# Kernel tuning notes

Measured on AMD Instinct MI355X. Metric: run time of the kernel, lower is better.

Reference implementation:

```python
import jax, jax.numpy as jnp
import numpy as np

N = 100000   # nodes
E = 1200000  # edges (avg degree 12)
F = 64       # hidden features

def setup_inputs() -> dict:
    key = jax.random.key(0)
    ks = jax.random.split(key, 10)
    x = jax.random.normal(ks[0], (N, F), dtype=jnp.float32)
    edge_src = jax.random.randint(ks[1], (E,), 0, N)
    edge_dst = jax.random.randint(ks[2], (E,), 0, N)
    edge_weights = jax.random.uniform(ks[3], (E,), dtype=jnp.float32)
    s = 1.0 / np.sqrt(F)
    W0 = jax.random.normal(ks[4], (F, F), dtype=jnp.float32) * s
    b0 = jnp.zeros((F,), dtype=jnp.float32)
    W1 = jax.random.normal(ks[5], (F, F), dtype=jnp.float32) * s
    b1 = jnp.zeros((F,), dtype=jnp.float32)
    W2 = jax.random.normal(ks[6], (F, 1), dtype=jnp.float32) * s
    b2 = jnp.zeros((1,), dtype=jnp.float32)
    return {"x": x, "edge_src": edge_src, "edge_dst": edge_dst,
            "edge_weights": edge_weights,
            "W0": W0, "b0": b0, "W1": W1, "b1": b1, "W2": W2, "b2": b2}

def reference(x, edge_src, edge_dst, edge_weights, W0, b0, W1, b1, W2, b2):
    n = x.shape[0]
    # GCN symmetric normalization with self loops (weight 1.0), as in pyg.nn.GCNConv
    deg = jax.ops.segment_sum(edge_weights, edge_dst, num_segments=n) + 1.0
    dinv = jax.lax.rsqrt(deg)                       # [N]
    norm = dinv[edge_src] * edge_weights * dinv[edge_dst]  # [E]
    self_norm = dinv * dinv                          # [N], self-loop coefficient

    def conv(h, W, b):
        h = h @ W                                    # linear transform first (PyG order)
        msg = h[edge_src] * norm[:, None]            # [E, F'] gather + scale
        agg = jax.ops.segment_sum(msg, edge_dst, num_segments=n)
        return agg + h * self_norm[:, None] + b

    h = jax.nn.relu(conv(x, W0, b0))
    h = jax.nn.relu(conv(h, W1, b1))
    h = conv(h, W2, b2)                              # [N, 1], no activation on last conv
    return jnp.squeeze(h)                            # [N]
```

## Files before the change

kernel.cpp:

```cpp
#include <hip/hip_runtime.h>

#define NN 100000
#define NE 1200000
#define FF 64
#define NBIN 512
#define BIN_NODES 196
#define BINCAP 2752
#define NTILE 6250
#define TPW 2

using bf16x8 = __attribute__((ext_vector_type(8))) short;
using f32x4  = __attribute__((ext_vector_type(4))) float;

__device__ __forceinline__ unsigned short f2bf(float x) {
    unsigned u = __float_as_uint(x);
    unsigned r = u + 0x7fffu + ((u >> 16) & 1u);
    return (unsigned short)(r >> 16);
}
__device__ __forceinline__ unsigned pack_bf2(float lo, float hi) {
    return (unsigned)f2bf(lo) | ((unsigned)f2bf(hi) << 16);
}
__device__ __forceinline__ float bf2f_lo(unsigned v) {
    return __uint_as_float(v << 16);
}
__device__ __forceinline__ float bf2f_hi(unsigned v) {
    return __uint_as_float(v & 0xffff0000u);
}

__global__ void zero_gptr(int* gptr) {
    gptr[threadIdx.x] = 0;
}

__global__ __launch_bounds__(1024) void bin_edges(
        const int* __restrict__ esrc, const int* __restrict__ edst,
        const float* __restrict__ ew, int* gptr, int2* __restrict__ binbuf, int e) {
    __shared__ int lcnt[NBIN];
    __shared__ int lbase[NBIN];
    int tid = threadIdx.x;
    int per = (e + (int)gridDim.x - 1) / (int)gridDim.x;
    int lo = blockIdx.x * per;
    int hi = min(lo + per, e);

    if (tid < NBIN) lcnt[tid] = 0;
    __syncthreads();

    for (int i = lo + tid; i < hi; i += 1024) {
        int b = (int)((unsigned)edst[i] / BIN_NODES);
        atomicAdd(&lcnt[b], 1);
    }
    __syncthreads();

    if (tid < NBIN) {
        int c = lcnt[tid];
        lbase[tid] = (c > 0) ? atomicAdd(&gptr[tid], c) : 0;
        lcnt[tid] = 0;
    }
    __syncthreads();

    for (int i = lo + tid; i < hi; i += 1024) {
        int d = edst[i];
        int b = (int)((unsigned)d / BIN_NODES);
        int s = atomicAdd(&lcnt[b], 1);
        int pos = lbase[b] + s;
        if (pos < BINCAP)
            binbuf[(size_t)b * BINCAP + pos] =
                make_int2(esrc[i] | ((d - b * BIN_NODES) << 17),
                          __float_as_int(ew[i]));
    }
}

__global__ __launch_bounds__(512) void build_compact(
        const int* __restrict__ gptr, const int2* __restrict__ binbuf,
        const float* __restrict__ x, int2* __restrict__ bucket,
        int* __restrict__ meta, float* __restrict__ dinv,
        uint4* __restrict__ t0, int n) {
    __shared__ int2  lbuck[BINCAP];
    __shared__ int   lc[BIN_NODES];
    __shared__ int   loff[BIN_NODES];
    __shared__ float ldeg[BIN_NODES];
    __shared__ int   sc[256];
    int b = blockIdx.x, tid = threadIdx.x;

    for (int i = tid; i < BIN_NODES; i += 512) { lc[i] = 0; ldeg[i] = 0.0f; }
    __syncthreads();

    int ce = min(gptr[b], BINCAP);
    const int2* bb = binbuf + (size_t)b * BINCAP;

    for (int i = tid; i < ce; i += 512) {
        int2 r = bb[i];
        int ln = (unsigned)r.x >> 17;
        atomicAdd(&lc[ln], 1);
        atomicAdd(&ldeg[ln], __int_as_float(r.y));
    }
    __syncthreads();

    if (tid < 256) sc[tid] = (tid < BIN_NODES) ? ((lc[tid] + 1) & ~1) : 0;
    __syncthreads();
#pragma unroll
    for (int s = 1; s < 256; s <<= 1) {
        int v = (tid < 256 && tid >= s) ? sc[tid - s] : 0;
        __syncthreads();
        if (tid < 256) sc[tid] += v;
        __syncthreads();
    }
    if (tid < BIN_NODES) loff[tid] = sc[tid] - ((lc[tid] + 1) & ~1);
    __syncthreads();
    int total = sc[BIN_NODES - 1];

    for (int i = tid; i < total; i += 512) lbuck[i] = make_int2(0, 0);
    __syncthreads();
    if (tid < BIN_NODES) lc[tid] = loff[tid];
    __syncthreads();

    for (int i = tid; i < ce; i += 512) {
        int2 r = bb[i];
        int ln = (unsigned)r.x >> 17;
        int pos = atomicAdd(&lc[ln], 1);
        lbuck[pos] = make_int2(r.x & 0x1FFFF, r.y);
    }
    __syncthreads();

    int gbase = b * BIN_NODES;
    for (int i = tid; i < BIN_NODES; i += 512) {
        float di = rsqrtf(ldeg[i] + 1.0f);
        int g = gbase + i;
        if (g < n) {
            dinv[g] = di;
            meta[g] = loff[i] | ((sc[i] - loff[i]) << 16);
        }
        ldeg[i] = di;
    }
    __syncthreads();

    {
        int lim4 = total >> 1;
        const int4* s4 = (const int4*)lbuck;
        int4* d4 = (int4*)(bucket + (size_t)b * BINCAP);
        for (int i = tid; i < lim4; i += 512) d4[i] = s4[i];
    }

    int eg = tid >> 3, l = tid & 7;
    for (int i = eg; i < BIN_NODES; i += 64) {
        int g = gbase + i;
        if (g >= n) continue;
        float di = ldeg[i];
        const float4* xp = (const float4*)(x + (size_t)g * FF + l * 8);
        float4 v0 = xp[0], v1 = xp[1];
        uint4 o;
        o.x = pack_bf2(v0.x * di, v0.y * di);
        o.y = pack_bf2(v0.z * di, v0.w * di);
        o.z = pack_bf2(v1.x * di, v1.y * di);
        o.w = pack_bf2(v1.z * di, v1.w * di);
        t0[(size_t)g * 8 + l] = o;
    }
}

__global__ __launch_bounds__(256) void agg8(
        const int* __restrict__ meta, const int4* __restrict__ bucket4,
        const uint4* __restrict__ t, const float* __restrict__ dinv,
        uint4* __restrict__ zb, int n) {
    int node = blockIdx.x * 32 + (threadIdx.x >> 3);
    int l = threadIdx.x & 7;
    if (node >= n) return;

    uint4 sv = t[node * 8 + l];
    float a0 = bf2f_lo(sv.x), a1 = bf2f_hi(sv.x);
    float a2 = bf2f_lo(sv.y), a3 = bf2f_hi(sv.y);
    float a4 = bf2f_lo(sv.z), a5 = bf2f_hi(sv.z);
    float a6 = bf2f_lo(sv.w), a7 = bf2f_hi(sv.w);

    int m = meta[node];
    int c = m >> 16;
    int bin = (int)((unsigned)node / BIN_NODES);
    const int4* bp = bucket4 + (((size_t)bin * BINCAP + (m & 0xFFFF)) >> 1);
    int p = 0;
    for (; p + 3 < c; p += 4) {
        int4 q0 = bp[(p >> 1) + 0];
        int4 q1 = bp[(p >> 1) + 1];
        uint4 v0 = t[q0.x * 8 + l];
        uint4 v1 = t[q0.z * 8 + l];
        uint4 v2 = t[q1.x * 8 + l];
        uint4 v3 = t[q1.z * 8 + l];
        float w0 = __int_as_float(q0.y), w1 = __int_as_float(q0.w);
        float w2 = __int_as_float(q1.y), w3 = __int_as_float(q1.w);
        a0 = fmaf(w0, bf2f_lo(v0.x), a0); a1 = fmaf(w0, bf2f_hi(v0.x), a1);
        a2 = fmaf(w0, bf2f_lo(v0.y), a2); a3 = fmaf(w0, bf2f_hi(v0.y), a3);
        a4 = fmaf(w0, bf2f_lo(v0.z), a4); a5 = fmaf(w0, bf2f_hi(v0.z), a5);
        a6 = fmaf(w0, bf2f_lo(v0.w), a6); a7 = fmaf(w0, bf2f_hi(v0.w), a7);
        a0 = fmaf(w1, bf2f_lo(v1.x), a0); a1 = fmaf(w1, bf2f_hi(v1.x), a1);
        a2 = fmaf(w1, bf2f_lo(v1.y), a2); a3 = fmaf(w1, bf2f_hi(v1.y), a3);
        a4 = fmaf(w1, bf2f_lo(v1.z), a4); a5 = fmaf(w1, bf2f_hi(v1.z), a5);
        a6 = fmaf(w1, bf2f_lo(v1.w), a6); a7 = fmaf(w1, bf2f_hi(v1.w), a7);
        a0 = fmaf(w2, bf2f_lo(v2.x), a0); a1 = fmaf(w2, bf2f_hi(v2.x), a1);
        a2 = fmaf(w2, bf2f_lo(v2.y), a2); a3 = fmaf(w2, bf2f_hi(v2.y), a3);
        a4 = fmaf(w2, bf2f_lo(v2.z), a4); a5 = fmaf(w2, bf2f_hi(v2.z), a5);
        a6 = fmaf(w2, bf2f_lo(v2.w), a6); a7 = fmaf(w2, bf2f_hi(v2.w), a7);
        a0 = fmaf(w3, bf2f_lo(v3.x), a0); a1 = fmaf(w3, bf2f_hi(v3.x), a1);
        a2 = fmaf(w3, bf2f_lo(v3.y), a2); a3 = fmaf(w3, bf2f_hi(v3.y), a3);
        a4 = fmaf(w3, bf2f_lo(v3.z), a4); a5 = fmaf(w3, bf2f_hi(v3.z), a5);
        a6 = fmaf(w3, bf2f_lo(v3.w), a6); a7 = fmaf(w3, bf2f_hi(v3.w), a7);
    }
    if (p < c) {
        int4 q0 = bp[p >> 1];
        uint4 v0 = t[q0.x * 8 + l];
        uint4 v1 = t[q0.z * 8 + l];
        float w0 = __int_as_float(q0.y), w1 = __int_as_float(q0.w);
        a0 = fmaf(w0, bf2f_lo(v0.x), a0); a1 = fmaf(w0, bf2f_hi(v0.x), a1);
        a2 = fmaf(w0, bf2f_lo(v0.y), a2); a3 = fmaf(w0, bf2f_hi(v0.y), a3);
        a4 = fmaf(w0, bf2f_lo(v0.z), a4); a5 = fmaf(w0, bf2f_hi(v0.z), a5);
        a6 = fmaf(w0, bf2f_lo(v0.w), a6); a7 = fmaf(w0, bf2f_hi(v0.w), a7);
        a0 = fmaf(w1, bf2f_lo(v1.x), a0); a1 = fmaf(w1, bf2f_hi(v1.x), a1);
        a2 = fmaf(w1, bf2f_lo(v1.y), a2); a3 = fmaf(w1, bf2f_hi(v1.y), a3);
        a4 = fmaf(w1, bf2f_lo(v1.z), a4); a5 = fmaf(w1, bf2f_hi(v1.z), a5);
        a6 = fmaf(w1, bf2f_lo(v1.w), a6); a7 = fmaf(w1, bf2f_hi(v1.w), a7);
    }
    float di = dinv[node];
    uint4 o;
    o.x = pack_bf2(a0 * di, a1 * di);
    o.y = pack_bf2(a2 * di, a3 * di);
    o.z = pack_bf2(a4 * di, a5 * di);
    o.w = pack_bf2(a6 * di, a7 * di);
    zb[node * 8 + l] = o;
}

__global__ __launch_bounds__(256) void gemmA(
        const unsigned short* __restrict__ zb, const float* __restrict__ W,
        const float* __restrict__ b, const float* __restrict__ dinv,
        unsigned short* __restrict__ t1, int ntiles) {
    int wid = blockIdx.x * 4 + (threadIdx.x >> 6);
    int lane = threadIdx.x & 63;
    int l16 = lane & 15, lg = lane >> 4;

    bf16x8 bf[4][2];
#pragma unroll
    for (int ct = 0; ct < 4; ++ct)
#pragma unroll
        for (int kh = 0; kh < 2; ++kh) {
            bf16x8 f;
#pragma unroll
            for (int j = 0; j < 8; ++j) {
                int k = kh * 32 + lg * 8 + j;
                f[j] = (short)f2bf(W[k * FF + ct * 16 + l16]);
            }
            bf[ct][kh] = f;
        }
    float bias_[4];
#pragma unroll
    for (int ct = 0; ct < 4; ++ct) bias_[ct] = b[ct * 16 + l16];

#pragma unroll
    for (int t = 0; t < TPW; ++t) {
        int tile = wid * TPW + t;
        if (tile >= ntiles) return;
        int rowbase = tile * 16;

        const bf16x8* zr = (const bf16x8*)(zb + (size_t)(rowbase + l16) * FF);
        bf16x8 a0 = zr[lg];
        bf16x8 a1 = zr[lg + 4];

        f32x4 acc[4];
#pragma unroll
        for (int ct = 0; ct < 4; ++ct) {
            acc[ct] = (f32x4){0.f, 0.f, 0.f, 0.f};
            acc[ct] = __builtin_amdgcn_mfma_f32_16x16x32_bf16(a0, bf[ct][0], acc[ct], 0, 0, 0);
            acc[ct] = __builtin_amdgcn_mfma_f32_16x16x32_bf16(a1, bf[ct][1], acc[ct], 0, 0, 0);
        }

        float dv[4];
#pragma unroll
        for (int r = 0; r < 4; ++r) dv[r] = dinv[rowbase + lg * 4 + r];
#pragma unroll
        for (int ct = 0; ct < 4; ++ct)
#pragma unroll
            for (int r = 0; r < 4; ++r) {
                float h = fmaxf(acc[ct][r] + bias_[ct], 0.0f) * dv[r];
                t1[(size_t)(rowbase + lg * 4 + r) * FF + ct * 16 + l16] = f2bf(h);
            }
    }
}

__global__ __launch_bounds__(256) void gemmB_tail(
        const unsigned short* __restrict__ zb, const float* __restrict__ W1,
        const float* __restrict__ b1, const float* __restrict__ W2,
        const float* __restrict__ dinv, float* __restrict__ t3, int ntiles) {
    int wid = blockIdx.x * 4 + (threadIdx.x >> 6);
    int lane = threadIdx.x & 63;
    int l16 = lane & 15, lg = lane >> 4;

    bf16x8 bf[4][2];
#pragma unroll
    for (int ct = 0; ct < 4; ++ct)
#pragma unroll
        for (int kh = 0; kh < 2; ++kh) {
            bf16x8 f;
#pragma unroll
            for (int j = 0; j < 8; ++j) {
                int k = kh * 32 + lg * 8 + j;
                f[j] = (short)f2bf(W1[k * FF + ct * 16 + l16]);
            }
            bf[ct][kh] = f;
        }
    float bias_[4], w2_[4];
#pragma unroll
    for (int ct = 0; ct < 4; ++ct) {
        bias_[ct] = b1[ct * 16 + l16];
        w2_[ct] = W2[ct * 16 + l16];
    }

#pragma unroll
    for (int t = 0; t < TPW; ++t) {
        int tile = wid * TPW + t;
        if (tile >= ntiles) return;
        int rowbase = tile * 16;

        const bf16x8* zr = (const bf16x8*)(zb + (size_t)(rowbase + l16) * FF);
        bf16x8 a0 = zr[lg];
        bf16x8 a1 = zr[lg + 4];

        f32x4 acc[4];
#pragma unroll
        for (int ct = 0; ct < 4; ++ct) {
            acc[ct] = (f32x4){0.f, 0.f, 0.f, 0.f};
            acc[ct] = __builtin_amdgcn_mfma_f32_16x16x32_bf16(a0, bf[ct][0], acc[ct], 0, 0, 0);
            acc[ct] = __builtin_amdgcn_mfma_f32_16x16x32_bf16(a1, bf[ct][1], acc[ct], 0, 0, 0);
        }

        float pr[4];
#pragma unroll
        for (int r = 0; r < 4; ++r) pr[r] = 0.0f;
#pragma unroll
        for (int ct = 0; ct < 4; ++ct)
#pragma unroll
            for (int r = 0; r < 4; ++r)
                pr[r] = fmaf(fmaxf(acc[ct][r] + bias_[ct], 0.0f), w2_[ct], pr[r]);
#pragma unroll
        for (int r = 0; r < 4; ++r) {
            pr[r] += __shfl_xor(pr[r], 1, 64);
            pr[r] += __shfl_xor(pr[r], 2, 64);
            pr[r] += __shfl_xor(pr[r], 4, 64);
            pr[r] += __shfl_xor(pr[r], 8, 64);
        }
        if (l16 == 0) {
#pragma unroll
            for (int r = 0; r < 4; ++r) {
                int row = rowbase + lg * 4 + r;
                t3[row] = pr[r] * dinv[row];
            }
        }
    }
}

__global__ __launch_bounds__(256) void final_out(
        const int* __restrict__ meta, const int2* __restrict__ bucket,
        const float* __restrict__ t3, const float* __restrict__ dinv,
        const float* __restrict__ b2, float* __restrict__ out, int n) {
    int node = blockIdx.x * 4 + (threadIdx.x >> 6);
    int lane = threadIdx.x & 63;
    if (node >= n) return;
    int m = meta[node];
    int c = m >> 16;
    int bin = (int)((unsigned)node / BIN_NODES);
    const int2* bp = bucket + (size_t)bin * BINCAP + (m & 0xFFFF);
    float v = 0.0f;
    for (int p = lane; p < c; p += 64) {
        int2 ed = bp[p];
        v = fmaf(__int_as_float(ed.y), t3[ed.x], v);
    }
#pragma unroll
    for (int off = 1; off < 64; off <<= 1) v += __shfl_xor(v, off, 64);
    if (lane == 0) out[node] = (v + t3[node]) * dinv[node] + b2[0];
}

extern "C" void kernel_launch(void* const* d_in, const int* in_sizes, int n_in,
                              void* d_out, int out_size, void* d_ws, size_t ws_size,
                              hipStream_t stream) {
    const float* x  = (const float*)d_in[0];
    const int* esrc = (const int*)d_in[1];
    const int* edst = (const int*)d_in[2];
    const float* ew = (const float*)d_in[3];
    const float* W0 = (const float*)d_in[4];
    const float* b0 = (const float*)d_in[5];
    const float* W1 = (const float*)d_in[6];
    const float* b1 = (const float*)d_in[7];
    const float* W2 = (const float*)d_in[8];
    const float* b2 = (const float*)d_in[9];
    float* out = (float*)d_out;

    const int n = NN, e = NE;

    char* ws = (char*)d_ws;
    size_t off = 0;
    auto alloc = [&](size_t bytes) {
        char* p = ws + off;
        off += (bytes + 255) & ~size_t(255);
        return p;
    };
    int*   meta   = (int*)  alloc(size_t(n) * 4);
    float* dinv   = (float*)alloc(size_t(n) * 4);
    float* t3     = (float*)alloc(size_t(n) * 4);
    int*   gptr   = (int*)  alloc(size_t(NBIN) * 4);
    int2*  bucket = (int2*) alloc(size_t(NBIN) * BINCAP * 8);
    unsigned short* zbuf = (unsigned short*)alloc(size_t(n) * FF * 2);
    unsigned short* t0   = (unsigned short*)alloc(size_t(n) * FF * 2);
    (void)ws_size;

    int2* binbuf = (int2*)zbuf;
    unsigned short* t1 = t0;

    int gN4  = (n + 3) / 4;
    int gN32 = (n + 31) / 32;
    int gGemm = ((NTILE + TPW - 1) / TPW + 3) / 4;

    zero_gptr<<<1, NBIN, 0, stream>>>(gptr);
    bin_edges<<<256, 1024, 0, stream>>>(esrc, edst, ew, gptr, binbuf, e);
    build_compact<<<NBIN, 512, 0, stream>>>(gptr, binbuf, x, bucket, meta, dinv,
                                            (uint4*)t0, n);
    agg8<<<gN32, 256, 0, stream>>>(meta, (const int4*)bucket, (const uint4*)t0,
                                   dinv, (uint4*)zbuf, n);
    gemmA<<<gGemm, 256, 0, stream>>>(zbuf, W0, b0, dinv, t1, NTILE);
    agg8<<<gN32, 256, 0, stream>>>(meta, (const int4*)bucket, (const uint4*)t1,
                                   dinv, (uint4*)zbuf, n);
    gemmB_tail<<<gGemm, 256, 0, stream>>>(zbuf, W1, b1, W2, dinv, t3, NTILE);
    final_out<<<gN4, 256, 0, stream>>>(meta, (const int2*)bucket, t3, dinv, b2, out, n);
}
```

Before: 134.3 us.

## Fuse neighbor aggregation with MFMA GEMM via shared-memory staging per block

```diff
diff --git a/kernel.cpp b/kernel.cpp
--- a/kernel.cpp
+++ b/kernel.cpp
@@ -6,8 +6,7 @@
 #define NBIN 512
 #define BIN_NODES 196
 #define BINCAP 2752
-#define NTILE 6250
-#define TPW 2
+#define LSTR 9
 
 using bf16x8 = __attribute__((ext_vector_type(8))) short;
 using f32x4  = __attribute__((ext_vector_type(4))) float;
@@ -156,15 +155,11 @@
     }
 }
 
-__global__ __launch_bounds__(256) void agg8(
+__device__ __forceinline__ void agg_node(
         const int* __restrict__ meta, const int4* __restrict__ bucket4,
         const uint4* __restrict__ t, const float* __restrict__ dinv,
-        uint4* __restrict__ zb, int n) {
-    int node = blockIdx.x * 32 + (threadIdx.x >> 3);
-    int l = threadIdx.x & 7;
-    if (node >= n) return;
-
-    uint4 sv = t[node * 8 + l];
+        int node, int l, uint4* __restrict__ ldsrow) {
+    uint4 sv = t[(size_t)node * 8 + l];
     float a0 = bf2f_lo(sv.x), a1 = bf2f_hi(sv.x);
     float a2 = bf2f_lo(sv.y), a3 = bf2f_hi(sv.y);
     float a4 = bf2f_lo(sv.z), a5 = bf2f_hi(sv.z);
@@ -221,132 +216,102 @@
     o.y = pack_bf2(a2 * di, a3 * di);
     o.z = pack_bf2(a4 * di, a5 * di);
     o.w = pack_bf2(a6 * di, a7 * di);
-    zb[node * 8 + l] = o;
-}
-
-__global__ __launch_bounds__(256) void gemmA(
-        const unsigned short* __restrict__ zb, const float* __restrict__ W,
-        const float* __restrict__ b, const float* __restrict__ dinv,
-        unsigned short* __restrict__ t1, int ntiles) {
-    int wid = blockIdx.x * 4 + (threadIdx.x >> 6);
-    int lane = threadIdx.x & 63;
+    ldsrow[l] = o;
+}
+
+__global__ __launch_bounds__(256) void fused_aggA(
+        const int* __restrict__ meta, const int4* __restrict__ bucket4,
+        const uint4* __restrict__ t, const float* __restrict__ dinv,
+        const float* __restrict__ W, const float* __restrict__ b,
+        unsigned short* __restrict__ t1) {
+    __shared__ uint4 lds[32 * LSTR];
+    int tid = threadIdx.x;
+    int r = tid >> 3, l = tid & 7;
+    int nodebase = blockIdx.x * 32;
+    agg_node(meta, bucket4, t, dinv, nodebase + r, l, &lds[r * LSTR]);
+    __syncthreads();
+
+    int wid = tid >> 6, lane = tid & 63;
+    if (wid >= 2) return;
     int l16 = lane & 15, lg = lane >> 4;
-
-    bf16x8 bf[4][2];
-#pragma unroll
-    for (int ct = 0; ct < 4; ++ct)
-#pragma unroll
-        for (int kh = 0; kh < 2; ++kh) {
-            bf16x8 f;
-#pragma unroll
-            for (int j = 0; j < 8; ++j) {
-                int k = kh * 32 + lg * 8 + j;
-                f[j] = (short)f2bf(W[k * FF + ct * 16 + l16]);
-            }
-            bf[ct][kh] = f;
-        }
-    float bias_[4];
-#pragma unroll
-    for (int ct = 0; ct < 4; ++ct) bias_[ct] = b[ct * 16 + l16];
-
-#pragma unroll
-    for (int t = 0; t < TPW; ++t) {
-        int tile = wid * TPW + t;
-        if (tile >= ntiles) return;
-        int rowbase = tile * 16;
-
-        const bf16x8* zr = (const bf16x8*)(zb + (size_t)(rowbase + l16) * FF);
-        bf16x8 a0 = zr[lg];
-        bf16x8 a1 = zr[lg + 4];
-
-        f32x4 acc[4];
-#pragma unroll
-        for (int ct = 0; ct < 4; ++ct) {
-            acc[ct] = (f32x4){0.f, 0.f, 0.f, 0.f};
-            acc[ct] = __builtin_amdgcn_mfma_f32_16x16x32_bf16(a0, bf[ct][0], acc[ct], 0, 0, 0);
-            acc[ct] = __builtin_amdgcn_mfma_f32_16x16x32_bf16(a1, bf[ct][1], acc[ct], 0, 0, 0);
-        }
-
-        float dv[4];
-#pragma unroll
-        for (int r = 0; r < 4; ++r) dv[r] = dinv[rowbase + lg * 4 + r];
-#pragma unroll
-        for (int ct = 0; ct < 4; ++ct)
-#pragma unroll
-            for (int r = 0; r < 4; ++r) {
-                float h = fmaxf(acc[ct][r] + bias_[ct], 0.0f) * dv[r];
-                t1[(size_t)(rowbase + lg * 4 + r) * FF + ct * 16 + l16] = f2bf(h);
-            }
-    }
-}
-
-__global__ __launch_bounds__(256) void gemmB_tail(
-        const unsigned short* __restrict__ zb, const float* __restrict__ W1,
-        const float* __restrict__ b1, const float* __restrict__ W2,
-        const float* __restrict__ dinv, float* __restrict__ t3, int ntiles) {
-    int wid = blockIdx.x * 4 + (threadIdx.x >> 6);
-    int lane = threadIdx.x & 63;
+    int rloc = wid * 16 + l16;
+    int rowbase = nodebase + wid * 16;
+
+    bf16x8 a0 = *(const bf16x8*)&lds[rloc * LSTR + lg];
+    bf16x8 a1 = *(const bf16x8*)&lds[rloc * LSTR + lg + 4];
+
+#pragma unroll
+    for (int ct = 0; ct < 4; ++ct) {
+        bf16x8 bf0, bf1;
+#pragma unroll
+        for (int j = 0; j < 8; ++j) {
+            bf0[j] = (short)f2bf(W[(lg * 8 + j) * FF + ct * 16 + l16]);
+            bf1[j] = (short)f2bf(W[(32 + lg * 8 + j) * FF + ct * 16 + l16]);
+        }
+        f32x4 acc = (f32x4){0.f, 0.f, 0.f, 0.f};
+        acc = __builtin_amdgcn_mfma_f32_16x16x32_bf16(a0, bf0, acc, 0, 0, 0);
+        acc = __builtin_amdgcn_mfma_f32_16x16x32_bf16(a1, bf1, acc, 0, 0, 0);
+        float bias_ = b[ct * 16 + l16];
+#pragma unroll
+        for (int rr = 0; rr < 4; ++rr) {
+            int row = rowbase + lg * 4 + rr;
+            float h = fmaxf(acc[rr] + bias_, 0.0f) * dinv[row];
+            t1[(size_t)row * FF + ct * 16 + l16] = f2bf(h);
+        }
+    }
+}
+
+__global__ __launch_bounds__(256) void fused_aggB(
+        const int* __restrict__ meta, const int4* __restrict__ bucket4,
+        const uint4* __restrict__ t, const float* __restrict__ dinv,
+        const float* __restrict__ W1, const float* __restrict__ b1,
+        const float* __restrict__ W2, float* __restrict__ t3) {
+    __shared__ uint4 lds[32 * LSTR];
+    int tid = threadIdx.x;
+    int r = tid >> 3, l = tid & 7;
+    int nodebase = blockIdx.x * 32;
+    agg_node(meta, bucket4, t, dinv, nodebase + r, l, &lds[r * LSTR]);
+    __syncthreads();
+
+    int wid = tid >> 6, lane = tid & 63;
+    if (wid >= 2) return;
     int l16 = lane & 15, lg = lane >> 4;
-
-    bf16x8 bf[4][2];
-#pragma unroll
-    for (int ct = 0; ct < 4; ++ct)
-#pragma unroll
-        for (int kh = 0; kh < 2; ++kh) {
-            bf16x8 f;
-#pragma unroll
-            for (int j = 0; j < 8; ++j) {
-                int k = kh * 32 + lg * 8 + j;
-                f[j] = (short)f2bf(W1[k * FF + ct * 16 + l16]);
-            }
-            bf[ct][kh] = f;
-        }
-    float bias_[4], w2_[4];
+    int rloc = wid * 16 + l16;
+    int rowbase = nodebase + wid * 16;
+
+    bf16x8 a0 = *(const bf16x8*)&lds[rloc * LSTR + lg];
+    bf16x8 a1 = *(const bf16x8*)&lds[rloc * LSTR + lg + 4];
+
+    float pr[4] = {0.f, 0.f, 0.f, 0.f};
 #pragma unroll
     for (int ct = 0; ct < 4; ++ct) {
-        bias_[ct] = b1[ct * 16 + l16];
-        w2_[ct] = W2[ct * 16 + l16];
-    }
-
-#pragma unroll
-    for (int t = 0; t < TPW; ++t) {
-        int tile = wid * TPW + t;
-        if (tile >= ntiles) return;
-        int rowbase = tile * 16;
-
-        const bf16x8* zr = (const bf16x8*)(zb + (size_t)(rowbase + l16) * FF);
-        bf16x8 a0 = zr[lg];
-        bf16x8 a1 = zr[lg + 4];
-
-        f32x4 acc[4];
-#pragma unroll
-        for (int ct = 0; ct < 4; ++ct) {
-            acc[ct] = (f32x4){0.f, 0.f, 0.f, 0.f};
-            acc[ct] = __builtin_amdgcn_mfma_f32_16x16x32_bf16(a0, bf[ct][0], acc[ct], 0, 0, 0);
-            acc[ct] = __builtin_amdgcn_mfma_f32_16x16x32_bf16(a1, bf[ct][1], acc[ct], 0, 0, 0);
-        }
-
-        float pr[4];
-#pragma unroll
-        for (int r = 0; r < 4; ++r) pr[r] = 0.0f;
-#pragma unroll
-        for (int ct = 0; ct < 4; ++ct)
-#pragma unroll
-            for (int r = 0; r < 4; ++r)
-                pr[r] = fmaf(fmaxf(acc[ct][r] + bias_[ct], 0.0f), w2_[ct], pr[r]);
-#pragma unroll
-        for (int r = 0; r < 4; ++r) {
-            pr[r] += __shfl_xor(pr[r], 1, 64);
-            pr[r] += __shfl_xor(pr[r], 2, 64);
-            pr[r] += __shfl_xor(pr[r], 4, 64);
-            pr[r] += __shfl_xor(pr[r], 8, 64);
-        }
-        if (l16 == 0) {
-#pragma unroll
-            for (int r = 0; r < 4; ++r) {
-                int row = rowbase + lg * 4 + r;
-                t3[row] = pr[r] * dinv[row];
-            }
+        bf16x8 bf0, bf1;
+#pragma unroll
+        for (int j = 0; j < 8; ++j) {
+            bf0[j] = (short)f2bf(W1[(lg * 8 + j) * FF + ct * 16 + l16]);
+            bf1[j] = (short)f2bf(W1[(32 + lg * 8 + j) * FF + ct * 16 + l16]);
+        }
+        f32x4 acc = (f32x4){0.f, 0.f, 0.f, 0.f};
+        acc = __builtin_amdgcn_mfma_f32_16x16x32_bf16(a0, bf0, acc, 0, 0, 0);
+        acc = __builtin_amdgcn_mfma_f32_16x16x32_bf16(a1, bf1, acc, 0, 0, 0);
+        float bias_ = b1[ct * 16 + l16];
+        float w2_ = W2[ct * 16 + l16];
+#pragma unroll
+        for (int rr = 0; rr < 4; ++rr)
+            pr[rr] = fmaf(fmaxf(acc[rr] + bias_, 0.0f), w2_, pr[rr]);
+    }
+#pragma unroll
+    for (int rr = 0; rr < 4; ++rr) {
+        pr[rr] += __shfl_xor(pr[rr], 1, 64);
+        pr[rr] += __shfl_xor(pr[rr], 2, 64);
+        pr[rr] += __shfl_xor(pr[rr], 4, 64);
+        pr[rr] += __shfl_xor(pr[rr], 8, 64);
+    }
+    if (l16 == 0) {
+#pragma unroll
+        for (int rr = 0; rr < 4; ++rr) {
+            int row = rowbase + lg * 4 + rr;
+            t3[row] = pr[rr] * dinv[row];
         }
     }
 }
@@ -406,21 +371,18 @@
     (void)ws_size;
 
     int2* binbuf = (int2*)zbuf;
-    unsigned short* t1 = t0;
-
-    int gN4  = (n + 3) / 4;
-    int gN32 = (n + 31) / 32;
-    int gGemm = ((NTILE + TPW - 1) / TPW + 3) / 4;
+    unsigned short* t1 = zbuf;
+
+    int gN4 = (n + 3) / 4;
+    int gFuse = n / 32;
 
     zero_gptr<<<1, NBIN, 0, stream>>>(gptr);
     bin_edges<<<256, 1024, 0, stream>>>(esrc, edst, ew, gptr, binbuf, e);
     build_compact<<<NBIN, 512, 0, stream>>>(gptr, binbuf, x, bucket, meta, dinv,
                                             (uint4*)t0, n);
-    agg8<<<gN32, 256, 0, stream>>>(meta, (const int4*)bucket, (const uint4*)t0,
-                                   dinv, (uint4*)zbuf, n);
-    gemmA<<<gGemm, 256, 0, stream>>>(zbuf, W0, b0, dinv, t1, NTILE);
-    agg8<<<gN32, 256, 0, stream>>>(meta, (const int4*)bucket, (const uint4*)t1,
-                                   dinv, (uint4*)zbuf, n);
-    gemmB_tail<<<gGemm, 256, 0, stream>>>(zbuf, W1, b1, W2, dinv, t3, NTILE);
+    fused_aggA<<<gFuse, 256, 0, stream>>>(meta, (const int4*)bucket,
+                                          (const uint4*)t0, dinv, W0, b0, t1);
+    fused_aggB<<<gFuse, 256, 0, stream>>>(meta, (const int4*)bucket,
+                                          (const uint4*)t1, dinv, W1, b1, W2, t3);
     final_out<<<gN4, 256, 0, stream>>>(meta, (const int2*)bucket, t3, dinv, b2, out, n);
 }
```

Result: faster. 124.5 us (-7.2%).
